# Kernel optimization log

Measured on AMD Instinct MI355X. Metric: run time of the kernel, lower is better.

The kernel has to match this reference:

```python
import jax, jax.numpy as jnp
import numpy as np

B, H, S, D = 2, 16, 2048, 64

def setup_inputs() -> dict:
    key = jax.random.key(0)
    kq, kk, kv = jax.random.split(key, 3)
    q = jax.random.normal(kq, (B, H, S, D), dtype=jnp.float32)
    k = jax.random.normal(kk, (B, H, S, D), dtype=jnp.float32)
    v = jax.random.normal(kv, (B, H, S, D), dtype=jnp.float32)
    # causal mask: True where position j > i (future tokens are masked)
    mask = jnp.triu(jnp.ones((S, S), dtype=bool), k=1)[None, None, :, :]
    return {"q": q, "k": k, "v": v, "mask": mask}

def reference(q, k, v, mask) -> jnp.ndarray:
    # scaled dot-product attention with additive -1e4 mask bias
    scale = 1.0 / jnp.sqrt(jnp.asarray(q.shape[-1], q.dtype))
    scores = jnp.einsum('bhqd,bhkd->bhqk', q, k) * scale  # [B,H,S,S]
    scores = scores + mask.astype(scores.dtype) * jnp.asarray(-10000.0, scores.dtype)
    probs = jax.nn.softmax(scores, axis=-1)
    # dropout is identity in eval mode
    return jnp.einsum('bhqk,bhkd->bhqd', probs, v)
```

## Files before the change

kernel.cpp:

```cpp
#include <hip/hip_runtime.h>

typedef __bf16 bf16_t;
typedef bf16_t bf16x2 __attribute__((ext_vector_type(2)));
typedef bf16_t bf16x8 __attribute__((ext_vector_type(8)));
typedef float  floatx16 __attribute__((ext_vector_type(16)));
typedef unsigned int uintx4 __attribute__((ext_vector_type(4)));

constexpr int Sq = 2048, Dq = 64;
constexpr int BQ = 64;
constexpr int KVB = 32;
constexpr int NQT = Sq / BQ;
constexpr float SCALE_LOG2E = 0.125f * 1.44269504088896340736f;
constexpr int KROW_B = 128;
constexpr int VROW_B = 80;

struct LoopS { char Kl[2][2][KVB * KROW_B]; char Vl[2][2][Dq * VROW_B]; };
struct EpiS  { float Op[BQ][Dq]; float den[BQ]; };
union  SmemU { LoopS l; EpiS e; };

static __device__ __forceinline__ bf16x8 cvt8(const float4& a, const float4& b) {
    bf16x8 w;
    w[0] = (bf16_t)a.x; w[1] = (bf16_t)a.y; w[2] = (bf16_t)a.z; w[3] = (bf16_t)a.w;
    w[4] = (bf16_t)b.x; w[5] = (bf16_t)b.y; w[6] = (bf16_t)b.z; w[7] = (bf16_t)b.w;
    return w;
}
static __device__ __forceinline__ bf16x8 cvt8s(const float4& a, const float4& b) {
    bf16x8 w;
    w[0] = (bf16_t)(a.x * SCALE_LOG2E); w[1] = (bf16_t)(a.y * SCALE_LOG2E);
    w[2] = (bf16_t)(a.z * SCALE_LOG2E); w[3] = (bf16_t)(a.w * SCALE_LOG2E);
    w[4] = (bf16_t)(b.x * SCALE_LOG2E); w[5] = (bf16_t)(b.y * SCALE_LOG2E);
    w[6] = (bf16_t)(b.z * SCALE_LOG2E); w[7] = (bf16_t)(b.w * SCALE_LOG2E);
    return w;
}
static __device__ __forceinline__ unsigned int pkbf(float lo, float hi) {
    bf16x2 t; t[0] = (bf16_t)lo; t[1] = (bf16_t)hi;
    return __builtin_bit_cast(unsigned int, t);
}

#define SUM16(p) (((((p)[0]+(p)[1])+((p)[2]+(p)[3]))+(((p)[4]+(p)[5])+((p)[6]+(p)[7]))) \
                + ((((p)[8]+(p)[9])+((p)[10]+(p)[11]))+(((p)[12]+(p)[13])+((p)[14]+(p)[15]))))

#define LOADKV(TG) do {                                                        \
    const long kb_ = base + (long)(TG) * KVB * Dq;                             \
    const float* kp_ = &K[kb_ + (long)krow_l * Dq + kc0];                      \
    kr0 = *(const float4*)&kp_[0];  kr1 = *(const float4*)&kp_[4];             \
    kr2 = *(const float4*)&kp_[8];  kr3 = *(const float4*)&kp_[12];            \
    const float* vp_ = &V[kb_ + (long)(16 * vkh) * Dq + vd];                   \
    _Pragma("unroll")                                                          \
    for (int m_ = 0; m_ < 16; ++m_) vraw[m_] = vp_[m_ * Dq];                   \
} while (0)

#define WRITEKV(BUF) do {                                                      \
    char* kc_ = &sm.l.Kl[grp][BUF][krow_l * KROW_B];                           \
    const int ksw_ = (krow_l & 7) << 4;                                        \
    *(bf16x8*)(kc_ + ((2 * kc0) ^ ksw_))      = cvt8(kr0, kr1);                \
    *(bf16x8*)(kc_ + ((2 * kc0 + 16) ^ ksw_)) = cvt8(kr2, kr3);                \
    char* vc_ = &sm.l.Vl[grp][BUF][vd * VROW_B + 32 * vkh];                    \
    bf16x8 v0_, v1_;                                                           \
    _Pragma("unroll")                                                          \
    for (int m_ = 0; m_ < 8; ++m_) {                                           \
        v0_[m_] = (bf16_t)vraw[m_]; v1_[m_] = (bf16_t)vraw[8 + m_];            \
    }                                                                          \
    *(bf16x8*)(vc_)      = v0_;                                                \
    *(bf16x8*)(vc_ + 16) = v1_;                                                \
} while (0)

__global__ __launch_bounds__(256, 2) void flash_attn_kernel(
    const float* __restrict__ Q, const float* __restrict__ K,
    const float* __restrict__ V, float* __restrict__ O)
{
    __shared__ SmemU sm;

    const int tid  = threadIdx.x;
    const int wave = tid >> 6;
    const int lane = tid & 63;
    const int hi   = lane >> 5;
    const int l31  = lane & 31;
    const int grp  = wave >> 1;
    const int qh   = wave & 1;

    const int id = blockIdx.x;
    const int bh = (id & 7) + ((id >> 7) << 3);
    const int pr = (id >> 3) & 15;
    const long base = (long)bh * Sq * Dq;

    const int gt     = tid & 127;
    const int krow_l = gt >> 2;
    const int kc0    = (gt & 3) * 16;
    const int vd     = gt >> 1;
    const int vkh    = gt & 1;

    for (int half = 0; half < 2; ++half) {
        const int qt = half ? (NQT - 1 - pr) : pr;
        const long qb = base + (long)qt * BQ * Dq;

        bf16x8 qf0, qf1, qf2, qf3;
        {
            const float* qp = &Q[qb + (long)(32 * qh + l31) * Dq + 8 * hi];
            qf0 = cvt8s(*(const float4*)&qp[0],  *(const float4*)&qp[4]);
            qf1 = cvt8s(*(const float4*)&qp[16], *(const float4*)&qp[20]);
            qf2 = cvt8s(*(const float4*)&qp[32], *(const float4*)&qp[36]);
            qf3 = cvt8s(*(const float4*)&qp[48], *(const float4*)&qp[52]);
        }

        float4 kr0, kr1, kr2, kr3;
        float  vraw[16];
        float  l_lane = 0.f;
        floatx16 oacc0 = (floatx16)0.f, oacc1 = (floatx16)0.f;

        __syncthreads();
        LOADKV(grp);
        WRITEKV(0);
        __syncthreads();

        for (int s = 0; s <= qt; ++s) {
            const int buf = s & 1;
            const bool more = (s < qt);
            if (more) LOADKV(2 * (s + 1) + grp);

            const int tg = 2 * s + grp;
            if (32 * tg <= 64 * qt + 32 * qh + 31) {
                const char* kb_ = &sm.l.Kl[grp][buf][l31 * KROW_B];
                const int lsw = (l31 & 7) << 4;

                floatx16 s0 = (floatx16)0.f;
                __builtin_amdgcn_s_setprio(1);
                s0 = __builtin_amdgcn_mfma_f32_32x32x16_bf16(
                         *(const bf16x8*)(kb_ + ((16 * hi) ^ lsw)),      qf0, s0, 0, 0, 0);
                s0 = __builtin_amdgcn_mfma_f32_32x32x16_bf16(
                         *(const bf16x8*)(kb_ + ((32 + 16 * hi) ^ lsw)), qf1, s0, 0, 0, 0);
                s0 = __builtin_amdgcn_mfma_f32_32x32x16_bf16(
                         *(const bf16x8*)(kb_ + ((64 + 16 * hi) ^ lsw)), qf2, s0, 0, 0, 0);
                s0 = __builtin_amdgcn_mfma_f32_32x32x16_bf16(
                         *(const bf16x8*)(kb_ + ((96 + 16 * hi) ^ lsw)), qf3, s0, 0, 0, 0);
                __builtin_amdgcn_s_setprio(0);

                float p0[16];
                const bool diag = (tg == 2 * qt + qh);
                #pragma unroll
                for (int r = 0; r < 16; ++r) {
                    const int cr = (r & 3) + 8 * (r >> 2) + 4 * hi;
                    float a = s0[r];
                    if (diag && (32 * tg + cr > 64 * qt + 32 * qh + l31)) a = -1e30f;
                    p0[r] = __builtin_amdgcn_exp2f(a);
                }
                l_lane += SUM16(p0);

                unsigned int w00, w01, w02, w03, w10, w11, w12, w13;
                {
                    unsigned int c0 = pkbf(p0[0], p0[1]), c1 = pkbf(p0[2], p0[3]);
                    unsigned int d0 = pkbf(p0[4], p0[5]), d1 = pkbf(p0[6], p0[7]);
                    asm volatile("v_permlane32_swap_b32 %0, %1" : "+v"(c0), "+v"(d0));
                    asm volatile("v_permlane32_swap_b32 %0, %1" : "+v"(c1), "+v"(d1));
                    w00 = c0; w01 = c1; w02 = d0; w03 = d1;
                }
                {
                    unsigned int c0 = pkbf(p0[8], p0[9]),   c1 = pkbf(p0[10], p0[11]);
                    unsigned int d0 = pkbf(p0[12], p0[13]), d1 = pkbf(p0[14], p0[15]);
                    asm volatile("v_permlane32_swap_b32 %0, %1" : "+v"(c0), "+v"(d0));
                    asm volatile("v_permlane32_swap_b32 %0, %1" : "+v"(c1), "+v"(d1));
                    w10 = c0; w11 = c1; w12 = d0; w13 = d1;
                }
                uintx4 f0; f0[0] = w00; f0[1] = w01; f0[2] = w02; f0[3] = w03;
                uintx4 f1; f1[0] = w10; f1[1] = w11; f1[2] = w12; f1[3] = w13;
                const bf16x8 pa0 = __builtin_bit_cast(bf16x8, f0);
                const bf16x8 pa1 = __builtin_bit_cast(bf16x8, f1);

                const char* vb_ = &sm.l.Vl[grp][buf][0];
                const char* vr0 = vb_ + l31 * VROW_B + 16 * hi;
                const char* vr1 = vb_ + (32 + l31) * VROW_B + 16 * hi;
                __builtin_amdgcn_s_setprio(1);
                oacc0 = __builtin_amdgcn_mfma_f32_32x32x16_bf16(
                            pa0, *(const bf16x8*)(vr0),      oacc0, 0, 0, 0);
                oacc0 = __builtin_amdgcn_mfma_f32_32x32x16_bf16(
                            pa1, *(const bf16x8*)(vr0 + 32), oacc0, 0, 0, 0);
                oacc1 = __builtin_amdgcn_mfma_f32_32x32x16_bf16(
                            pa0, *(const bf16x8*)(vr1),      oacc1, 0, 0, 0);
                oacc1 = __builtin_amdgcn_mfma_f32_32x32x16_bf16(
                            pa1, *(const bf16x8*)(vr1 + 32), oacc1, 0, 0, 0);
                __builtin_amdgcn_s_setprio(0);
            }

            if (more) WRITEKV(buf ^ 1);
            __syncthreads();
        }

        const float lden = l_lane + __shfl_xor(l_lane, 32);

        if (grp == 1) {
            #pragma unroll
            for (int r = 0; r < 16; ++r) {
                const int cr = (r & 3) + 8 * (r >> 2) + 4 * hi;
                sm.e.Op[32 * qh + cr][l31]      = oacc0[r];
                sm.e.Op[32 * qh + cr][32 + l31] = oacc1[r];
            }
            if (hi == 0) sm.e.den[32 * qh + l31] = lden;
        }
        __syncthreads();
        if (grp == 0) {
            #pragma unroll
            for (int r = 0; r < 16; ++r) {
                const int cr = (r & 3) + 8 * (r >> 2) + 4 * hi;
                const float dA = __shfl(lden, cr);
                const float dB = sm.e.den[32 * qh + cr];
                const float inv = 1.f / (dA + dB);
                const long orow = qb + (long)(32 * qh + cr) * Dq;
                O[orow + l31]      = (oacc0[r] + sm.e.Op[32 * qh + cr][l31]) * inv;
                O[orow + 32 + l31] = (oacc1[r] + sm.e.Op[32 * qh + cr][32 + l31]) * inv;
            }
        }
    }
}

extern "C" void kernel_launch(void* const* d_in, const int* in_sizes, int n_in,
                              void* d_out, int out_size, void* d_ws, size_t ws_size,
                              hipStream_t stream)
{
    const float* q = (const float*)d_in[0];
    const float* k = (const float*)d_in[1];
    const float* v = (const float*)d_in[2];
    float* out = (float*)d_out;
    flash_attn_kernel<<<dim3(512, 1, 1), dim3(256, 1, 1), 0, stream>>>(q, k, v, out);
}
```

Baseline: 147.6 us.

## Drop LDS staging, load K/V directly into registers with 32-row query tiles

Replaces the shared-memory double-buffered K/V pipeline with per-wave direct global loads of K and V into MFMA operand registers. Each block now handles one 32-row query tile with two waves that split the KV tiles, launching 2048 blocks of 128 threads instead of 512 blocks that each processed a paired pair of 64-row tiles. This removes LDS writes, reads and per-step barriers, at the cost of V loads becoming strided scalar gathers and K/V being fetched separately by each wave and block with no reuse across query rows.

New measurement: 219.1 us. 1.48x slower.

```diff
diff --git a/kernel.cpp b/kernel.cpp
--- a/kernel.cpp
+++ b/kernel.cpp
@@ -7,16 +7,12 @@
 typedef unsigned int uintx4 __attribute__((ext_vector_type(4)));
 
 constexpr int Sq = 2048, Dq = 64;
-constexpr int BQ = 64;
+constexpr int QW = 32;
 constexpr int KVB = 32;
-constexpr int NQT = Sq / BQ;
+constexpr int NT = Sq / QW;
 constexpr float SCALE_LOG2E = 0.125f * 1.44269504088896340736f;
-constexpr int KROW_B = 128;
-constexpr int VROW_B = 80;
 
-struct LoopS { char Kl[2][2][KVB * KROW_B]; char Vl[2][2][Dq * VROW_B]; };
-struct EpiS  { float Op[BQ][Dq]; float den[BQ]; };
-union  SmemU { LoopS l; EpiS e; };
+struct Smem { float Op[QW][Dq]; float den[QW]; };
 
 static __device__ __forceinline__ bf16x8 cvt8(const float4& a, const float4& b) {
     bf16x8 w;
@@ -40,174 +36,134 @@
 #define SUM16(p) (((((p)[0]+(p)[1])+((p)[2]+(p)[3]))+(((p)[4]+(p)[5])+((p)[6]+(p)[7]))) \
                 + ((((p)[8]+(p)[9])+((p)[10]+(p)[11]))+(((p)[12]+(p)[13])+((p)[14]+(p)[15]))))
 
-#define LOADKV(TG) do {                                                        \
-    const long kb_ = base + (long)(TG) * KVB * Dq;                             \
-    const float* kp_ = &K[kb_ + (long)krow_l * Dq + kc0];                      \
-    kr0 = *(const float4*)&kp_[0];  kr1 = *(const float4*)&kp_[4];             \
-    kr2 = *(const float4*)&kp_[8];  kr3 = *(const float4*)&kp_[12];            \
-    const float* vp_ = &V[kb_ + (long)(16 * vkh) * Dq + vd];                   \
-    _Pragma("unroll")                                                          \
-    for (int m_ = 0; m_ < 16; ++m_) vraw[m_] = vp_[m_ * Dq];                   \
-} while (0)
-
-#define WRITEKV(BUF) do {                                                      \
-    char* kc_ = &sm.l.Kl[grp][BUF][krow_l * KROW_B];                           \
-    const int ksw_ = (krow_l & 7) << 4;                                        \
-    *(bf16x8*)(kc_ + ((2 * kc0) ^ ksw_))      = cvt8(kr0, kr1);                \
-    *(bf16x8*)(kc_ + ((2 * kc0 + 16) ^ ksw_)) = cvt8(kr2, kr3);                \
-    char* vc_ = &sm.l.Vl[grp][BUF][vd * VROW_B + 32 * vkh];                    \
-    bf16x8 v0_, v1_;                                                           \
-    _Pragma("unroll")                                                          \
-    for (int m_ = 0; m_ < 8; ++m_) {                                           \
-        v0_[m_] = (bf16_t)vraw[m_]; v1_[m_] = (bf16_t)vraw[8 + m_];            \
-    }                                                                          \
-    *(bf16x8*)(vc_)      = v0_;                                                \
-    *(bf16x8*)(vc_ + 16) = v1_;                                                \
-} while (0)
-
-__global__ __launch_bounds__(256, 2) void flash_attn_kernel(
+__global__ __launch_bounds__(128, 4) void flash_attn_kernel(
     const float* __restrict__ Q, const float* __restrict__ K,
     const float* __restrict__ V, float* __restrict__ O)
 {
-    __shared__ SmemU sm;
+    __shared__ Smem sm;
 
     const int tid  = threadIdx.x;
-    const int wave = tid >> 6;
+    const int grp  = tid >> 6;
     const int lane = tid & 63;
     const int hi   = lane >> 5;
     const int l31  = lane & 31;
-    const int grp  = wave >> 1;
-    const int qh   = wave & 1;
 
     const int id = blockIdx.x;
-    const int bh = (id & 7) + ((id >> 7) << 3);
-    const int pr = (id >> 3) & 15;
+    const int g  = id >> 3;
+    const int bh = (id & 7) + ((g >> 6) << 3);
+    const int m  = g & 63;
+    const int j  = (m & 1) ? (NT - 1 - (m >> 1)) : (m >> 1);
     const long base = (long)bh * Sq * Dq;
+    const long qb   = base + (long)j * QW * Dq;
 
-    const int gt     = tid & 127;
-    const int krow_l = gt >> 2;
-    const int kc0    = (gt & 3) * 16;
-    const int vd     = gt >> 1;
-    const int vkh    = gt & 1;
+    bf16x8 qf0, qf1, qf2, qf3;
+    {
+        const float* qp = &Q[qb + (long)l31 * Dq + 8 * hi];
+        qf0 = cvt8s(*(const float4*)&qp[0],  *(const float4*)&qp[4]);
+        qf1 = cvt8s(*(const float4*)&qp[16], *(const float4*)&qp[20]);
+        qf2 = cvt8s(*(const float4*)&qp[32], *(const float4*)&qp[36]);
+        qf3 = cvt8s(*(const float4*)&qp[48], *(const float4*)&qp[52]);
+    }
 
-    for (int half = 0; half < 2; ++half) {
-        const int qt = half ? (NQT - 1 - pr) : pr;
-        const long qb = base + (long)qt * BQ * Dq;
+    float l_lane = 0.f;
+    floatx16 oacc0 = (floatx16)0.f, oacc1 = (floatx16)0.f;
 
-        bf16x8 qf0, qf1, qf2, qf3;
-        {
-            const float* qp = &Q[qb + (long)(32 * qh + l31) * Dq + 8 * hi];
-            qf0 = cvt8s(*(const float4*)&qp[0],  *(const float4*)&qp[4]);
-            qf1 = cvt8s(*(const float4*)&qp[16], *(const float4*)&qp[20]);
-            qf2 = cvt8s(*(const float4*)&qp[32], *(const float4*)&qp[36]);
-            qf3 = cvt8s(*(const float4*)&qp[48], *(const float4*)&qp[52]);
+    for (int t = grp; t <= j; t += 2) {
+        const long kb = base + (long)t * KVB * Dq;
+
+        const float* kp = &K[kb + (long)l31 * Dq + 8 * hi];
+        const float4 k00 = *(const float4*)&kp[0],  k01 = *(const float4*)&kp[4];
+        const float4 k10 = *(const float4*)&kp[16], k11 = *(const float4*)&kp[20];
+        const float4 k20 = *(const float4*)&kp[32], k21 = *(const float4*)&kp[36];
+        const float4 k30 = *(const float4*)&kp[48], k31 = *(const float4*)&kp[52];
+
+        const float* vp = &V[kb + (long)(8 * hi) * Dq];
+        float va[16], vb[16];
+        #pragma unroll
+        for (int jj = 0; jj < 8; ++jj) {
+            va[jj]     = vp[jj * Dq + l31];
+            va[8 + jj] = vp[(16 + jj) * Dq + l31];
+            vb[jj]     = vp[jj * Dq + 32 + l31];
+            vb[8 + jj] = vp[(16 + jj) * Dq + 32 + l31];
         }
 
-        float4 kr0, kr1, kr2, kr3;
-        float  vraw[16];
-        float  l_lane = 0.f;
-        floatx16 oacc0 = (floatx16)0.f, oacc1 = (floatx16)0.f;
+        const bf16x8 kf0 = cvt8(k00, k01), kf1 = cvt8(k10, k11);
+        const bf16x8 kf2 = cvt8(k20, k21), kf3 = cvt8(k30, k31);
+        floatx16 s0 = (floatx16)0.f;
+        __builtin_amdgcn_s_setprio(1);
+        s0 = __builtin_amdgcn_mfma_f32_32x32x16_bf16(kf0, qf0, s0, 0, 0, 0);
+        s0 = __builtin_amdgcn_mfma_f32_32x32x16_bf16(kf1, qf1, s0, 0, 0, 0);
+        s0 = __builtin_amdgcn_mfma_f32_32x32x16_bf16(kf2, qf2, s0, 0, 0, 0);
+        s0 = __builtin_amdgcn_mfma_f32_32x32x16_bf16(kf3, qf3, s0, 0, 0, 0);
+        __builtin_amdgcn_s_setprio(0);
 
-        __syncthreads();
-        LOADKV(grp);
-        WRITEKV(0);
-        __syncthreads();
+        float p0[16];
+        const bool diag = (t == j);
+        #pragma unroll
+        for (int r = 0; r < 16; ++r) {
+            const int cr = (r & 3) + 8 * (r >> 2) + 4 * hi;
+            float a = s0[r];
+            if (diag && (cr > l31)) a = -1e30f;
+            p0[r] = __builtin_amdgcn_exp2f(a);
+        }
+        l_lane += SUM16(p0);
 
-        for (int s = 0; s <= qt; ++s) {
-            const int buf = s & 1;
-            const bool more = (s < qt);
-            if (more) LOADKV(2 * (s + 1) + grp);
+        unsigned int w00, w01, w02, w03, w10, w11, w12, w13;
+        {
+            unsigned int c0 = pkbf(p0[0], p0[1]), c1 = pkbf(p0[2], p0[3]);
+            unsigned int d0 = pkbf(p0[4], p0[5]), d1 = pkbf(p0[6], p0[7]);
+            asm volatile("v_permlane32_swap_b32 %0, %1" : "+v"(c0), "+v"(d0));
+            asm volatile("v_permlane32_swap_b32 %0, %1" : "+v"(c1), "+v"(d1));
+            w00 = c0; w01 = c1; w02 = d0; w03 = d1;
+        }
+        {
+            unsigned int c0 = pkbf(p0[8], p0[9]),   c1 = pkbf(p0[10], p0[11]);
+            unsigned int d0 = pkbf(p0[12], p0[13]), d1 = pkbf(p0[14], p0[15]);
+            asm volatile("v_permlane32_swap_b32 %0, %1" : "+v"(c0), "+v"(d0));
+            asm volatile("v_permlane32_swap_b32 %0, %1" : "+v"(c1), "+v"(d1));
+            w10 = c0; w11 = c1; w12 = d0; w13 = d1;
+        }
+        uintx4 f0; f0[0] = w00; f0[1] = w01; f0[2] = w02; f0[3] = w03;
+        uintx4 f1; f1[0] = w10; f1[1] = w11; f1[2] = w12; f1[3] = w13;
+        const bf16x8 pa0 = __builtin_bit_cast(bf16x8, f0);
+        const bf16x8 pa1 = __builtin_bit_cast(bf16x8, f1);
 
-            const int tg = 2 * s + grp;
-            if (32 * tg <= 64 * qt + 32 * qh + 31) {
-                const char* kb_ = &sm.l.Kl[grp][buf][l31 * KROW_B];
-                const int lsw = (l31 & 7) << 4;
+        bf16x8 vf00, vf01, vf10, vf11;
+        #pragma unroll
+        for (int jj = 0; jj < 8; ++jj) {
+            vf00[jj] = (bf16_t)va[jj];     vf01[jj] = (bf16_t)va[8 + jj];
+            vf10[jj] = (bf16_t)vb[jj];     vf11[jj] = (bf16_t)vb[8 + jj];
+        }
+        __builtin_amdgcn_s_setprio(1);
+        oacc0 = __builtin_amdgcn_mfma_f32_32x32x16_bf16(pa0, vf00, oacc0, 0, 0, 0);
+        oacc0 = __builtin_amdgcn_mfma_f32_32x32x16_bf16(pa1, vf01, oacc0, 0, 0, 0);
+        oacc1 = __builtin_amdgcn_mfma_f32_32x32x16_bf16(pa0, vf10, oacc1, 0, 0, 0);
+        oacc1 = __builtin_amdgcn_mfma_f32_32x32x16_bf16(pa1, vf11, oacc1, 0, 0, 0);
+        __builtin_amdgcn_s_setprio(0);
+    }
 
-                floatx16 s0 = (floatx16)0.f;
-                __builtin_amdgcn_s_setprio(1);
-                s0 = __builtin_amdgcn_mfma_f32_32x32x16_bf16(
-                         *(const bf16x8*)(kb_ + ((16 * hi) ^ lsw)),      qf0, s0, 0, 0, 0);
-                s0 = __builtin_amdgcn_mfma_f32_32x32x16_bf16(
-                         *(const bf16x8*)(kb_ + ((32 + 16 * hi) ^ lsw)), qf1, s0, 0, 0, 0);
-                s0 = __builtin_amdgcn_mfma_f32_32x32x16_bf16(
-                         *(const bf16x8*)(kb_ + ((64 + 16 * hi) ^ lsw)), qf2, s0, 0, 0, 0);
-                s0 = __builtin_amdgcn_mfma_f32_32x32x16_bf16(
-                         *(const bf16x8*)(kb_ + ((96 + 16 * hi) ^ lsw)), qf3, s0, 0, 0, 0);
-                __builtin_amdgcn_s_setprio(0);
+    const float lden = l_lane + __shfl_xor(l_lane, 32);
 
-                float p0[16];
-                const bool diag = (tg == 2 * qt + qh);
-                #pragma unroll
-                for (int r = 0; r < 16; ++r) {
-                    const int cr = (r & 3) + 8 * (r >> 2) + 4 * hi;
-                    float a = s0[r];
-                    if (diag && (32 * tg + cr > 64 * qt + 32 * qh + l31)) a = -1e30f;
-                    p0[r] = __builtin_amdgcn_exp2f(a);
-                }
-                l_lane += SUM16(p0);
-
-                unsigned int w00, w01, w02, w03, w10, w11, w12, w13;
-                {
-                    unsigned int c0 = pkbf(p0[0], p0[1]), c1 = pkbf(p0[2], p0[3]);
-                    unsigned int d0 = pkbf(p0[4], p0[5]), d1 = pkbf(p0[6], p0[7]);
-                    asm volatile("v_permlane32_swap_b32 %0, %1" : "+v"(c0), "+v"(d0));
-                    asm volatile("v_permlane32_swap_b32 %0, %1" : "+v"(c1), "+v"(d1));
-                    w00 = c0; w01 = c1; w02 = d0; w03 = d1;
-                }
-                {
-                    unsigned int c0 = pkbf(p0[8], p0[9]),   c1 = pkbf(p0[10], p0[11]);
-                    unsigned int d0 = pkbf(p0[12], p0[13]), d1 = pkbf(p0[14], p0[15]);
-                    asm volatile("v_permlane32_swap_b32 %0, %1" : "+v"(c0), "+v"(d0));
-                    asm volatile("v_permlane32_swap_b32 %0, %1" : "+v"(c1), "+v"(d1));
-                    w10 = c0; w11 = c1; w12 = d0; w13 = d1;
-                }
-                uintx4 f0; f0[0] = w00; f0[1] = w01; f0[2] = w02; f0[3] = w03;
-                uintx4 f1; f1[0] = w10; f1[1] = w11; f1[2] = w12; f1[3] = w13;
-                const bf16x8 pa0 = __builtin_bit_cast(bf16x8, f0);
-                const bf16x8 pa1 = __builtin_bit_cast(bf16x8, f1);
-
-                const char* vb_ = &sm.l.Vl[grp][buf][0];
-                const char* vr0 = vb_ + l31 * VROW_B + 16 * hi;
-                const char* vr1 = vb_ + (32 + l31) * VROW_B + 16 * hi;
-                __builtin_amdgcn_s_setprio(1);
-                oacc0 = __builtin_amdgcn_mfma_f32_32x32x16_bf16(
-                            pa0, *(const bf16x8*)(vr0),      oacc0, 0, 0, 0);
-                oacc0 = __builtin_amdgcn_mfma_f32_32x32x16_bf16(
-                            pa1, *(const bf16x8*)(vr0 + 32), oacc0, 0, 0, 0);
-                oacc1 = __builtin_amdgcn_mfma_f32_32x32x16_bf16(
-                            pa0, *(const bf16x8*)(vr1),      oacc1, 0, 0, 0);
-                oacc1 = __builtin_amdgcn_mfma_f32_32x32x16_bf16(
-                            pa1, *(const bf16x8*)(vr1 + 32), oacc1, 0, 0, 0);
-                __builtin_amdgcn_s_setprio(0);
-            }
-
-            if (more) WRITEKV(buf ^ 1);
-            __syncthreads();
+    if (grp == 1) {
+        #pragma unroll
+        for (int r = 0; r < 16; ++r) {
+            const int cr = (r & 3) + 8 * (r >> 2) + 4 * hi;
+            sm.Op[cr][l31]      = oacc0[r];
+            sm.Op[cr][32 + l31] = oacc1[r];
         }
-
-        const float lden = l_lane + __shfl_xor(l_lane, 32);
-
-        if (grp == 1) {
-            #pragma unroll
-            for (int r = 0; r < 16; ++r) {
-                const int cr = (r & 3) + 8 * (r >> 2) + 4 * hi;
-                sm.e.Op[32 * qh + cr][l31]      = oacc0[r];
-                sm.e.Op[32 * qh + cr][32 + l31] = oacc1[r];
-            }
-            if (hi == 0) sm.e.den[32 * qh + l31] = lden;
-        }
-        __syncthreads();
-        if (grp == 0) {
-            #pragma unroll
-            for (int r = 0; r < 16; ++r) {
-                const int cr = (r & 3) + 8 * (r >> 2) + 4 * hi;
-                const float dA = __shfl(lden, cr);
-                const float dB = sm.e.den[32 * qh + cr];
-                const float inv = 1.f / (dA + dB);
-                const long orow = qb + (long)(32 * qh + cr) * Dq;
-                O[orow + l31]      = (oacc0[r] + sm.e.Op[32 * qh + cr][l31]) * inv;
-                O[orow + 32 + l31] = (oacc1[r] + sm.e.Op[32 * qh + cr][32 + l31]) * inv;
-            }
+        if (hi == 0) sm.den[l31] = lden;
+    }
+    __syncthreads();
+    if (grp == 0) {
+        #pragma unroll
+        for (int r = 0; r < 16; ++r) {
+            const int cr = (r & 3) + 8 * (r >> 2) + 4 * hi;
+            const float dA = __shfl(lden, cr);
+            const float dB = sm.den[cr];
+            const float inv = 1.f / (dA + dB);
+            const long orow = qb + (long)cr * Dq;
+            O[orow + l31]      = (oacc0[r] + sm.Op[cr][l31]) * inv;
+            O[orow + 32 + l31] = (oacc1[r] + sm.Op[cr][32 + l31]) * inv;
         }
     }
 }
@@ -220,5 +176,5 @@
     const float* k = (const float*)d_in[1];
     const float* v = (const float*)d_in[2];
     float* out = (float*)d_out;
-    flash_attn_kernel<<<dim3(512, 1, 1), dim3(256, 1, 1), 0, stream>>>(q, k, v, out);
+    flash_attn_kernel<<<dim3(2048, 1, 1), dim3(128, 1, 1), 0, stream>>>(q, k, v, out);
 }
```
